# Kernel optimization log

Hardware: AMD Instinct MI355X
Metric: run time of the kernel (lower is better)

The kernel has to match this reference:

```python
import jax, jax.numpy as jnp
import numpy as np

D_CONV = 4  # matches Mamba(d_conv=4)


def _silu(v):
    return v * jax.nn.sigmoid(v)


def _mamba_block(x, in_w, cw, cb, xw, dtw, dtb, A_log, Dp, ow):
    # x: (B, L, d_model)
    B, L, _ = x.shape
    d_inner, d_state = A_log.shape
    xz = x @ in_w.T                        # (B, L, 2*d_inner)
    xr, z = jnp.split(xz, 2, axis=-1)      # each (B, L, d_inner)
    # causal depthwise conv1d (pad d_conv-1 on the left, truncate to L)
    xp = jnp.pad(xr, ((0, 0), (D_CONV - 1, 0), (0, 0)))
    xc = sum(xp[:, k:k + L, :] * cw[:, k] for k in range(D_CONV)) + cb
    xc = _silu(xc)                         # (B, L, d_inner)
    dbl = xc @ xw.T                        # (B, L, dt_rank + 2*d_state)
    dt_rank = dbl.shape[-1] - 2 * d_state
    dt, Bm, Cm = jnp.split(dbl, [dt_rank, dt_rank + d_state], axis=-1)
    dt = jax.nn.softplus(dt @ dtw.T + dtb)  # (B, L, d_inner)
    A = -jnp.exp(A_log)                    # (d_inner, d_state)
    dA = jnp.exp(dt[..., None] * A)                          # (B, L, d_inner, d_state)
    dBx = dt[..., None] * Bm[:, :, None, :] * xc[..., None]  # (B, L, d_inner, d_state)

    def step(h, inputs):
        dA_t, dBx_t, C_t = inputs          # (B,d,s), (B,d,s), (B,s)
        h = dA_t * h + dBx_t
        y = jnp.einsum('bds,bs->bd', h, C_t)
        return h, y

    h0 = jnp.zeros((B, d_inner, d_state), x.dtype)
    _, ys = jax.lax.scan(step, h0, (dA.transpose(1, 0, 2, 3),
                                    dBx.transpose(1, 0, 2, 3),
                                    Cm.transpose(1, 0, 2)))
    y = ys.transpose(1, 0, 2) + xc * Dp    # skip term D*u
    y = y * _silu(z)                       # gated
    return y @ ow.T                        # (B, L, d_model)


def setup_inputs() -> dict:
    key = jax.random.key(0)
    d_model, d_state, n_layer = 1024, 16, 2
    d_inner = 2 * d_model
    dt_rank = d_model // 16  # ceil(1024/16)
    Bsz, L = 2, 1024
    ks = jax.random.split(key, 8)
    s = 0.02
    x = jax.random.normal(ks[0], (Bsz, L, d_model), jnp.float32)
    in_proj_w = jax.random.normal(ks[1], (n_layer, 2 * d_inner, d_model), jnp.float32) * s
    conv_w = jax.random.normal(ks[2], (n_layer, d_inner, D_CONV), jnp.float32) * 0.2
    conv_b = jnp.zeros((n_layer, d_inner), jnp.float32)
    x_proj_w = jax.random.normal(ks[3], (n_layer, dt_rank + 2 * d_state, d_inner), jnp.float32) * s
    dt_proj_w = jax.random.normal(ks[4], (n_layer, d_inner, dt_rank), jnp.float32) * s
    dt_proj_b = jax.random.uniform(ks[5], (n_layer, d_inner), jnp.float32, -5.0, -3.0)
    A_log = jnp.log(jnp.tile(jnp.arange(1, d_state + 1, dtype=jnp.float32), (n_layer, d_inner, 1)))
    D = jnp.ones((n_layer, d_inner), jnp.float32)
    out_proj_w = jax.random.normal(ks[6], (n_layer, d_model, d_inner), jnp.float32) * s
    return {"x": x, "in_proj_w": in_proj_w, "conv_w": conv_w, "conv_b": conv_b,
            "x_proj_w": x_proj_w, "dt_proj_w": dt_proj_w, "dt_proj_b": dt_proj_b,
            "A_log": A_log, "D": D, "out_proj_w": out_proj_w}


def reference(x, in_proj_w, conv_w, conv_b, x_proj_w, dt_proj_w, dt_proj_b, A_log, D, out_proj_w):
    n_layer = in_proj_w.shape[0]
    for i in range(n_layer):
        x = _mamba_block(x, in_proj_w[i], conv_w[i], conv_b[i], x_proj_w[i],
                         dt_proj_w[i], dt_proj_b[i], A_log[i], D[i], out_proj_w[i])
    return x
```

## Files before the change

kernel.cpp:

```cpp
#include <hip/hip_runtime.h>
#include <hip/hip_bf16.h>
#include <cmath>

typedef __bf16 bf16x8_t __attribute__((ext_vector_type(8)));
typedef float  f32x4_t  __attribute__((ext_vector_type(4)));
using bf16 = __hip_bfloat16;

#define LOG2E 1.44269504088896340736f
#define LN2   0.69314718055994530942f

#define AS1C(p) ((const __attribute__((address_space(1))) void*)(p))
#define AS3C(p) ((__attribute__((address_space(3))) void*)(p))

__device__ __forceinline__ float fexp2(float x) { return __builtin_amdgcn_exp2f(x); }
__device__ __forceinline__ float flog2(float x) { return __builtin_amdgcn_logf(x); }
__device__ __forceinline__ float frcp (float x) { return __builtin_amdgcn_rcpf(x); }

__global__ __launch_bounds__(256)
void cast_multi(const float* s0, bf16* d0, int e0,
                const float* s1, bf16* d1, int e1,
                const float* s2, bf16* d2, int e2,
                const float* s3, bf16* d3, int e3,
                const float* s4, bf16* d4, int e4)
{
    const int blk = blockIdx.x;
    const float* src; bf16* dst; int base;
    if      (blk < e0) { src = s0; dst = d0; base = blk; }
    else if (blk < e1) { src = s1; dst = d1; base = blk - e0; }
    else if (blk < e2) { src = s2; dst = d2; base = blk - e1; }
    else if (blk < e3) { src = s3; dst = d3; base = blk - e2; }
    else               { src = s4; dst = d4; base = blk - e3; }

    const int i = base * 256 + threadIdx.x;
    const float4* s = (const float4*)(src + (size_t)i * 8);
    float4 a = s[0], b = s[1];
    bf16 o[8];
    o[0] = __float2bfloat16(a.x); o[1] = __float2bfloat16(a.y);
    o[2] = __float2bfloat16(a.z); o[3] = __float2bfloat16(a.w);
    o[4] = __float2bfloat16(b.x); o[5] = __float2bfloat16(b.y);
    o[6] = __float2bfloat16(b.z); o[7] = __float2bfloat16(b.w);
    *(int4*)(dst + (size_t)i * 8) = *(int4*)o;
}

template<int MODE, bool SPLITK>
__global__ __launch_bounds__(256)
void gemm_bf16(const bf16* __restrict__ A, const bf16* __restrict__ B,
               float* __restrict__ Cf, bf16* __restrict__ Cb,
               int M, int N, int K, int lda, int ldb, int ldc)
{
    __shared__ __align__(16) bf16 At[2][128][32];
    __shared__ __align__(16) bf16 Bt[2][128][32];

    const int tid  = threadIdx.x;
    const int lane = tid & 63;
    const int wid  = tid >> 6;
    const int wr   = wid >> 1;
    const int wc   = wid & 1;
    const int fr   = lane & 15;
    const int fq   = lane >> 4;

    const int row0 = blockIdx.y * 128;
    const int col0 = blockIdx.x * 128;
    const int kb   = SPLITK ? blockIdx.z * K : 0;

    const int g_row = wid * 32 + (lane >> 2);
    const int g_kp  = (lane & 3) * 8;
    const bf16* aP0 = A + (size_t)(row0 + g_row) * lda + g_kp + kb;
    const bf16* aP1 = A + (size_t)(row0 + g_row + 16) * lda + g_kp + kb;
    int bR0 = col0 + g_row;      if (bR0 >= N) bR0 = N - 1;
    int bR1 = col0 + g_row + 16; if (bR1 >= N) bR1 = N - 1;
    const bf16* bP0 = B + (size_t)bR0 * ldb + g_kp + kb;
    const bf16* bP1 = B + (size_t)bR1 * ldb + g_kp + kb;

    f32x4_t acc[4][4];
    #pragma unroll
    for (int m = 0; m < 4; ++m)
        #pragma unroll
        for (int n = 0; n < 4; ++n)
            acc[m][n] = f32x4_t{0.f, 0.f, 0.f, 0.f};

    auto STAGE = [&](int buf, int k0) {
        __builtin_amdgcn_global_load_lds(AS1C(aP0 + k0), AS3C(&At[buf][wid * 32][0]),      16, 0, 0);
        __builtin_amdgcn_global_load_lds(AS1C(aP1 + k0), AS3C(&At[buf][wid * 32 + 16][0]), 16, 0, 0);
        __builtin_amdgcn_global_load_lds(AS1C(bP0 + k0), AS3C(&Bt[buf][wid * 32][0]),      16, 0, 0);
        __builtin_amdgcn_global_load_lds(AS1C(bP1 + k0), AS3C(&Bt[buf][wid * 32 + 16][0]), 16, 0, 0);
    };

    STAGE(0, 0);
    __syncthreads();
    int cur = 0;
    for (int k0 = 0; k0 < K; k0 += 32) {
        if (k0 + 32 < K) STAGE(cur ^ 1, k0 + 32);

        bf16x8_t af[4], bg[4];
        #pragma unroll
        for (int m = 0; m < 4; ++m)
            af[m] = *(const bf16x8_t*)&At[cur][wr * 64 + m * 16 + fr][fq * 8];
        #pragma unroll
        for (int n = 0; n < 4; ++n)
            bg[n] = *(const bf16x8_t*)&Bt[cur][wc * 64 + n * 16 + fr][fq * 8];
        #pragma unroll
        for (int m = 0; m < 4; ++m)
            #pragma unroll
            for (int n = 0; n < 4; ++n)
                acc[m][n] = __builtin_amdgcn_mfma_f32_16x16x32_bf16(
                    af[m], bg[n], acc[m][n], 0, 0, 0);

        __syncthreads();
        cur ^= 1;
    }

    float* Cfz = SPLITK ? (Cf + (size_t)blockIdx.z * M * ldc) : Cf;

    #pragma unroll
    for (int m = 0; m < 4; ++m) {
        #pragma unroll
        for (int n = 0; n < 4; ++n) {
            const int c = col0 + wc * 64 + n * 16 + fr;
            if (c < N) {
                #pragma unroll
                for (int r = 0; r < 4; ++r) {
                    const int rr = row0 + wr * 64 + m * 16 + fq * 4 + r;
                    if (SPLITK || MODE != 1) Cfz[(size_t)rr * ldc + c] = acc[m][n][r];
                    if (!SPLITK && MODE != 0) Cb[(size_t)rr * ldc + c] = __float2bfloat16(acc[m][n][r]);
                }
            }
        }
    }
}

__global__ __launch_bounds__(256)
void reduce_pk(const float* __restrict__ part, float* __restrict__ of,
               bf16* __restrict__ oh, int n4, int stride4, int S)
{
    const int i = blockIdx.x * blockDim.x + threadIdx.x;
    if (i >= n4) return;
    const float4* p4 = (const float4*)part;
    float4 s = p4[i];
    for (int k = 1; k < S; ++k) {
        float4 v = p4[(size_t)k * stride4 + i];
        s.x += v.x; s.y += v.y; s.z += v.z; s.w += v.w;
    }
    if (of) ((float4*)of)[i] = s;
    if (oh) {
        bf16 o[4];
        o[0] = __float2bfloat16(s.x); o[1] = __float2bfloat16(s.y);
        o[2] = __float2bfloat16(s.z); o[3] = __float2bfloat16(s.w);
        *(int2*)(oh + (size_t)i * 4) = *(int2*)o;
    }
}

__global__ __launch_bounds__(256)
void conv_silu(const bf16* __restrict__ xz, const float* __restrict__ cw,
               const float* __restrict__ cb, bf16* __restrict__ xc,
               int Bsz, int L, int dinner)
{
    const int nv = dinner / 4;
    const int g  = blockIdx.x * blockDim.x + threadIdx.x;
    const int d4 = (g % nv) * 4;
    const int t  = (g / nv) % L;
    const int b  = g / (nv * L);
    if (b >= Bsz) return;

    const int ldxz = 2 * dinner;
    float4 w0 = *(const float4*)(cw + (size_t)(d4 + 0) * 4);
    float4 w1 = *(const float4*)(cw + (size_t)(d4 + 1) * 4);
    float4 w2 = *(const float4*)(cw + (size_t)(d4 + 2) * 4);
    float4 w3 = *(const float4*)(cw + (size_t)(d4 + 3) * 4);
    float4 acc = *(const float4*)(cb + d4);

    const bf16* base = xz + (size_t)b * L * ldxz + d4;
    #pragma unroll
    for (int k = 0; k < 4; ++k) {
        const int ts = t - 3 + k;
        if (ts >= 0) {
            const bf16* rp = base + (size_t)ts * ldxz;
            float vx = __bfloat162float(rp[0]);
            float vy = __bfloat162float(rp[1]);
            float vz = __bfloat162float(rp[2]);
            float vw = __bfloat162float(rp[3]);
            acc.x = fmaf(vx, (&w0.x)[k], acc.x);
            acc.y = fmaf(vy, (&w1.x)[k], acc.y);
            acc.z = fmaf(vz, (&w2.x)[k], acc.z);
            acc.w = fmaf(vw, (&w3.x)[k], acc.w);
        }
    }
    acc.x = acc.x * frcp(1.f + fexp2(-acc.x * LOG2E));
    acc.y = acc.y * frcp(1.f + fexp2(-acc.y * LOG2E));
    acc.z = acc.z * frcp(1.f + fexp2(-acc.z * LOG2E));
    acc.w = acc.w * frcp(1.f + fexp2(-acc.w * LOG2E));

    bf16 o[4];
    o[0] = __float2bfloat16(acc.x); o[1] = __float2bfloat16(acc.y);
    o[2] = __float2bfloat16(acc.z); o[3] = __float2bfloat16(acc.w);
    *(int2*)(xc + ((size_t)b * L + t) * dinner + d4) = *(int2*)o;
}

__global__ __launch_bounds__(256)
void scan_part1(const bf16* __restrict__ dtraw, const bf16* __restrict__ xc,
                const float* __restrict__ dbl, const float* __restrict__ dtb,
                const float* __restrict__ alog, float* __restrict__ hend,
                float* __restrict__ Ssum, int Bsz, int L, int dinner,
                int NC, int CL)
{
    const int g  = blockIdx.x * blockDim.x + threadIdx.x;
    const int sq = g & 3;
    const int d  = (g >> 2) % dinner;
    const int c  = ((g >> 2) / dinner) % NC;
    const int b  = g / (4 * dinner * NC);
    if (b >= Bsz) return;

    float4 av = *(const float4*)(alog + (size_t)d * 16 + sq * 4);
    const float As0 = -fexp2(av.x * LOG2E) * LOG2E;
    const float As1 = -fexp2(av.y * LOG2E) * LOG2E;
    const float As2 = -fexp2(av.z * LOG2E) * LOG2E;
    const float As3 = -fexp2(av.w * LOG2E) * LOG2E;
    const float bias = dtb[d];

    const int t0 = c * CL;
    const bf16*  dt_p = dtraw + ((size_t)b * L + t0) * dinner + d;
    const bf16*  xc_p = xc    + ((size_t)b * L + t0) * dinner + d;
    const float* bl_p = dbl   + ((size_t)b * L + t0) * 96 + 64 + sq * 4;

    float h0 = 0.f, h1 = 0.f, h2 = 0.f, h3 = 0.f, S = 0.f;
    for (int t = 0; t < CL; ++t) {
        const float dtv = __bfloat162float(*dt_p);
        const float xcv = __bfloat162float(*xc_p);
        const float4 Bv = *(const float4*)bl_p;

        const float xv = dtv + bias;
        const float e  = fexp2(xv * LOG2E);
        const float sp = (xv > 15.f) ? xv : LN2 * flog2(1.f + e);
        S += sp;
        const float u = sp * xcv;
        h0 = fmaf(fexp2(sp * As0), h0, u * Bv.x);
        h1 = fmaf(fexp2(sp * As1), h1, u * Bv.y);
        h2 = fmaf(fexp2(sp * As2), h2, u * Bv.z);
        h3 = fmaf(fexp2(sp * As3), h3, u * Bv.w);

        dt_p += dinner; xc_p += dinner; bl_p += 96;
    }

    const size_t idx = ((size_t)b * NC + c) * dinner + d;
    *(float4*)(hend + idx * 16 + sq * 4) = make_float4(h0, h1, h2, h3);
    if (sq == 0) Ssum[idx] = S;
}

__global__ __launch_bounds__(256)
void scan_part2(bf16* dty, const bf16* __restrict__ xc,
                const float* __restrict__ dbl, const bf16* __restrict__ xz,
                const float* __restrict__ dtb, const float* __restrict__ alog,
                const float* __restrict__ Dp, const float* __restrict__ hend,
                const float* __restrict__ Ssum,
                int Bsz, int L, int dinner, int NC, int CL)
{
    const int g  = blockIdx.x * blockDim.x + threadIdx.x;
    const int sq = g & 3;
    const int d  = (g >> 2) % dinner;
    const int c  = ((g >> 2) / dinner) % NC;
    const int b  = g / (4 * dinner * NC);
    if (b >= Bsz) return;

    float4 av = *(const float4*)(alog + (size_t)d * 16 + sq * 4);
    const float As0 = -fexp2(av.x * LOG2E) * LOG2E;
    const float As1 = -fexp2(av.y * LOG2E) * LOG2E;
    const float As2 = -fexp2(av.z * LOG2E) * LOG2E;
    const float As3 = -fexp2(av.w * LOG2E) * LOG2E;
    const float bias = dtb[d];
    const float Dval = Dp[d];

    float h0 = 0.f, h1 = 0.f, h2 = 0.f, h3 = 0.f;
    for (int cp = 0; cp < c; ++cp) {
        const size_t idx = ((size_t)b * NC + cp) * dinner + d;
        const float4 he = *(const float4*)(hend + idx * 16 + sq * 4);
        const float  Sv = Ssum[idx];
        h0 = fmaf(fexp2(As0 * Sv), h0, he.x);
        h1 = fmaf(fexp2(As1 * Sv), h1, he.y);
        h2 = fmaf(fexp2(As2 * Sv), h2, he.z);
        h3 = fmaf(fexp2(As3 * Sv), h3, he.w);
    }

    const int t0 = c * CL;
    bf16*        dt_p = dty + ((size_t)b * L + t0) * dinner + d;
    const bf16*  xc_p = xc  + ((size_t)b * L + t0) * dinner + d;
    const float* bl_p = dbl + ((size_t)b * L + t0) * 96 + 64 + sq * 4;
    const bf16*  z_p  = xz  + ((size_t)b * L + t0) * (2 * dinner) + dinner + d;

    for (int t = 0; t < CL; ++t) {
        const float dtv = __bfloat162float(*dt_p);
        const float xcv = __bfloat162float(*xc_p);
        const float4 Bv = *(const float4*)bl_p;
        const float4 Cv = *(const float4*)(bl_p + 16);
        const float zv  = __bfloat162float(*z_p);

        const float xv = dtv + bias;
        const float e  = fexp2(xv * LOG2E);
        const float sp = (xv > 15.f) ? xv : LN2 * flog2(1.f + e);
        const float u = sp * xcv;
        h0 = fmaf(fexp2(sp * As0), h0, u * Bv.x);
        h1 = fmaf(fexp2(sp * As1), h1, u * Bv.y);
        h2 = fmaf(fexp2(sp * As2), h2, u * Bv.z);
        h3 = fmaf(fexp2(sp * As3), h3, u * Bv.w);

        float y = h0 * Cv.x + h1 * Cv.y + h2 * Cv.z + h3 * Cv.w;
        y += __shfl_xor(y, 1, 4);
        y += __shfl_xor(y, 2, 4);

        if (sq == 0) {
            y = fmaf(xcv, Dval, y);
            const float sig = frcp(1.f + fexp2(-zv * LOG2E));
            *dt_p = __float2bfloat16(y * (zv * sig));
        }

        dt_p += dinner; xc_p += dinner; bl_p += 96; z_p += 2 * dinner;
    }
}

extern "C" void kernel_launch(void* const* d_in, const int* in_sizes, int n_in,
                              void* d_out, int out_size, void* d_ws, size_t ws_size,
                              hipStream_t stream)
{
    const float* x    = (const float*)d_in[0];
    const float* inw  = (const float*)d_in[1];
    const float* cw   = (const float*)d_in[2];
    const float* cb   = (const float*)d_in[3];
    const float* xw   = (const float*)d_in[4];
    const float* dtw  = (const float*)d_in[5];
    const float* dtb  = (const float*)d_in[6];
    const float* alog = (const float*)d_in[7];
    const float* Dp   = (const float*)d_in[8];
    const float* ow   = (const float*)d_in[9];
    float* out = (float*)d_out;

    const int Bsz = 2, L = 1024, dmodel = 1024, dinner = 2048;
    const int BL = Bsz * L;
    const int NC = 32, CL = L / NC;
    const int SPX = 16, KSX = dinner / SPX;
    const int SPO = 2,  KSO = dinner / SPO;

    char* p = (char*)d_ws;
    auto alloc = [&](size_t bytes) { char* r = p; p += (bytes + 63) & ~size_t(63); return r; };
    bf16*  wb_in  = (bf16*) alloc((size_t)2 * 2 * dinner * dmodel * 2);
    bf16*  wb_x   = (bf16*) alloc((size_t)2 * 96 * dinner * 2);
    bf16*  wb_dt  = (bf16*) alloc((size_t)2 * dinner * 64 * 2);
    bf16*  wb_ow  = (bf16*) alloc((size_t)2 * dmodel * dinner * 2);
    bf16*  curb   = (bf16*) alloc((size_t)BL * dmodel * 2);
    bf16*  xzb16  = (bf16*) alloc((size_t)BL * 2 * dinner * 2);
    bf16*  xcb16  = (bf16*) alloc((size_t)BL * dinner * 2);
    float* dblb   = (float*)alloc((size_t)BL * 96 * 4);
    bf16*  dblb16 = (bf16*) alloc((size_t)BL * 96 * 2);
    bf16*  dtrb16 = (bf16*) alloc((size_t)BL * dinner * 2);
    float* hendb  = (float*)alloc((size_t)Bsz * NC * dinner * 16 * 4);
    float* ssumb  = (float*)alloc((size_t)Bsz * NC * dinner * 4);
    float* partb  = (float*)alloc((size_t)SPO * BL * dmodel * 4);

    const int scan_blocks = (Bsz * NC * dinner * 4) / 256;

    {
        const int n8_x  = BL * dmodel / 8;
        const int n8_in = 2 * 2 * dinner * dmodel / 8;
        const int n8_xw = 2 * 96 * dinner / 8;
        const int n8_dt = 2 * dinner * 64 / 8;
        const int n8_ow = 2 * dmodel * dinner / 8;
        const int e0 = n8_x / 256;
        const int e1 = e0 + n8_in / 256;
        const int e2 = e1 + n8_xw / 256;
        const int e3 = e2 + n8_dt / 256;
        const int e4 = e3 + n8_ow / 256;
        cast_multi<<<e4, 256, 0, stream>>>(
            x, curb, e0, inw, wb_in, e1, xw, wb_x, e2, dtw, wb_dt, e3, ow, wb_ow, e4);
    }

    for (int l = 0; l < 2; ++l) {
        const bf16*  wb_in_l = wb_in + (size_t)l * 2 * dinner * dmodel;
        const bf16*  wb_x_l  = wb_x  + (size_t)l * 96 * dinner;
        const bf16*  wb_dt_l = wb_dt + (size_t)l * dinner * 64;
        const bf16*  wb_ow_l = wb_ow + (size_t)l * dmodel * dinner;
        const float* cw_l    = cw   + (size_t)l * dinner * 4;
        const float* cb_l    = cb   + (size_t)l * dinner;
        const float* dtb_l   = dtb  + (size_t)l * dinner;
        const float* alog_l  = alog + (size_t)l * dinner * 16;
        const float* Dp_l    = Dp   + (size_t)l * dinner;

        gemm_bf16<1, false><<<dim3(2 * dinner / 128, BL / 128), 256, 0, stream>>>(
            curb, wb_in_l, nullptr, xzb16, BL, 2 * dinner, dmodel, dmodel, dmodel, 2 * dinner);

        conv_silu<<<(BL * dinner / 4) / 256, 256, 0, stream>>>(
            xzb16, cw_l, cb_l, xcb16, Bsz, L, dinner);

        gemm_bf16<0, true><<<dim3(1, BL / 128, SPX), 256, 0, stream>>>(
            xcb16, wb_x_l, partb, nullptr, BL, 96, KSX, dinner, dinner, 96);
        reduce_pk<<<(BL * 96 / 4 + 255) / 256, 256, 0, stream>>>(
            partb, dblb, dblb16, BL * 96 / 4, BL * 96 / 4, SPX);

        gemm_bf16<1, false><<<dim3(dinner / 128, BL / 128), 256, 0, stream>>>(
            dblb16, wb_dt_l, nullptr, dtrb16, BL, dinner, 64, 96, 64, dinner);

        scan_part1<<<scan_blocks, 256, 0, stream>>>(
            dtrb16, xcb16, dblb, dtb_l, alog_l, hendb, ssumb, Bsz, L, dinner, NC, CL);
        scan_part2<<<scan_blocks, 256, 0, stream>>>(
            dtrb16, xcb16, dblb, xzb16, dtb_l, alog_l, Dp_l, hendb, ssumb,
            Bsz, L, dinner, NC, CL);

        gemm_bf16<0, true><<<dim3(dmodel / 128, BL / 128, SPO), 256, 0, stream>>>(
            dtrb16, wb_ow_l, partb, nullptr, BL, dmodel, KSO, dinner, dinner, dmodel);
        if (l == 0)
            reduce_pk<<<(BL * dmodel / 4 + 255) / 256, 256, 0, stream>>>(
                partb, nullptr, curb, BL * dmodel / 4, BL * dmodel / 4, SPO);
        else
            reduce_pk<<<(BL * dmodel / 4 + 255) / 256, 256, 0, stream>>>(
                partb, out, nullptr, BL * dmodel / 4, BL * dmodel / 4, SPO);
    }
}
```

Before: 331.4 us.

## Swizzle GEMM LDS tiles and add separate chunk-prefix kernel for scan

Two changes. First, the bf16 GEMM's LDS layout gets an XOR swizzle on the 8-element k-chunk, applied both where global_load_lds writes and where MFMA fragments are read, so LDS bank conflicts drop. Second, each scan_part2 thread used to walk every preceding chunk's end state itself, which is quadratic work in the chunk count. A new chunk_prefix kernel now computes the exclusive prefix of chunk states once and writes it in place over hend, and scan_part2 reads its initial state directly. This costs an extra kernel launch and a serial pass over NC per (b,d,s) lane.

```diff
diff --git a/kernel.cpp b/kernel.cpp
--- a/kernel.cpp
+++ b/kernel.cpp
@@ -64,7 +64,7 @@
     const int kb   = SPLITK ? blockIdx.z * K : 0;
 
     const int g_row = wid * 32 + (lane >> 2);
-    const int g_kp  = (lane & 3) * 8;
+    const int g_kp  = (((lane & 3) ^ ((lane >> 3) & 3)) * 8);
     const bf16* aP0 = A + (size_t)(row0 + g_row) * lda + g_kp + kb;
     const bf16* aP1 = A + (size_t)(row0 + g_row + 16) * lda + g_kp + kb;
     int bR0 = col0 + g_row;      if (bR0 >= N) bR0 = N - 1;
@@ -72,6 +72,8 @@
     const bf16* bP0 = B + (size_t)bR0 * ldb + g_kp + kb;
     const bf16* bP1 = B + (size_t)bR1 * ldb + g_kp + kb;
 
+    const int rchunk = (fq ^ ((fr >> 1) & 3)) * 8;
+
     f32x4_t acc[4][4];
     #pragma unroll
     for (int m = 0; m < 4; ++m)
@@ -95,10 +97,10 @@
         bf16x8_t af[4], bg[4];
         #pragma unroll
         for (int m = 0; m < 4; ++m)
-            af[m] = *(const bf16x8_t*)&At[cur][wr * 64 + m * 16 + fr][fq * 8];
+            af[m] = *(const bf16x8_t*)&At[cur][wr * 64 + m * 16 + fr][rchunk];
         #pragma unroll
         for (int n = 0; n < 4; ++n)
-            bg[n] = *(const bf16x8_t*)&Bt[cur][wc * 64 + n * 16 + fr][fq * 8];
+            bg[n] = *(const bf16x8_t*)&Bt[cur][wc * 64 + n * 16 + fr][rchunk];
         #pragma unroll
         for (int m = 0; m < 4; ++m)
             #pragma unroll
@@ -247,11 +249,32 @@
 }
 
 __global__ __launch_bounds__(256)
+void chunk_prefix(float* __restrict__ hend, const float* __restrict__ Ssum,
+                  const float* __restrict__ alog, int Bsz, int dinner, int NC)
+{
+    const int g = blockIdx.x * blockDim.x + threadIdx.x;
+    const int s = g & 15;
+    const int d = (g >> 4) % dinner;
+    const int b = g / (16 * dinner);
+    if (b >= Bsz) return;
+
+    const float As2 = -fexp2(alog[(size_t)d * 16 + s] * LOG2E) * LOG2E;
+
+    float h = 0.f;
+    for (int c = 0; c < NC; ++c) {
+        const size_t idx = ((size_t)b * NC + c) * dinner + d;
+        const float he = hend[idx * 16 + s];
+        const float Sv = Ssum[idx];
+        hend[idx * 16 + s] = h;
+        h = fmaf(fexp2(As2 * Sv), h, he);
+    }
+}
+
+__global__ __launch_bounds__(256)
 void scan_part2(bf16* dty, const bf16* __restrict__ xc,
                 const float* __restrict__ dbl, const bf16* __restrict__ xz,
                 const float* __restrict__ dtb, const float* __restrict__ alog,
-                const float* __restrict__ Dp, const float* __restrict__ hend,
-                const float* __restrict__ Ssum,
+                const float* __restrict__ Dp, const float* __restrict__ hinit,
                 int Bsz, int L, int dinner, int NC, int CL)
 {
     const int g  = blockIdx.x * blockDim.x + threadIdx.x;
@@ -269,16 +292,9 @@
     const float bias = dtb[d];
     const float Dval = Dp[d];
 
-    float h0 = 0.f, h1 = 0.f, h2 = 0.f, h3 = 0.f;
-    for (int cp = 0; cp < c; ++cp) {
-        const size_t idx = ((size_t)b * NC + cp) * dinner + d;
-        const float4 he = *(const float4*)(hend + idx * 16 + sq * 4);
-        const float  Sv = Ssum[idx];
-        h0 = fmaf(fexp2(As0 * Sv), h0, he.x);
-        h1 = fmaf(fexp2(As1 * Sv), h1, he.y);
-        h2 = fmaf(fexp2(As2 * Sv), h2, he.z);
-        h3 = fmaf(fexp2(As3 * Sv), h3, he.w);
-    }
+    const size_t cidx = ((size_t)b * NC + c) * dinner + d;
+    float4 hv = *(const float4*)(hinit + cidx * 16 + sq * 4);
+    float h0 = hv.x, h1 = hv.y, h2 = hv.z, h3 = hv.w;
 
     const int t0 = c * CL;
     bf16*        dt_p = dty + ((size_t)b * L + t0) * dinner + d;
@@ -355,6 +371,7 @@
     float* partb  = (float*)alloc((size_t)SPO * BL * dmodel * 4);
 
     const int scan_blocks = (Bsz * NC * dinner * 4) / 256;
+    const int pfx_blocks  = (Bsz * dinner * 16) / 256;
 
     {
         const int n8_x  = BL * dmodel / 8;
@@ -398,8 +415,10 @@
 
         scan_part1<<<scan_blocks, 256, 0, stream>>>(
             dtrb16, xcb16, dblb, dtb_l, alog_l, hendb, ssumb, Bsz, L, dinner, NC, CL);
+        chunk_prefix<<<pfx_blocks, 256, 0, stream>>>(
+            hendb, ssumb, alog_l, Bsz, dinner, NC);
         scan_part2<<<scan_blocks, 256, 0, stream>>>(
-            dtrb16, xcb16, dblb, xzb16, dtb_l, alog_l, Dp_l, hendb, ssumb,
+            dtrb16, xcb16, dblb, xzb16, dtb_l, alog_l, Dp_l, hendb,
             Bsz, L, dinner, NC, CL);
 
         gemm_bf16<0, true><<<dim3(dmodel / 128, BL / 128, SPO), 256, 0, stream>>>(
```

Result: no change. 332.6 us (+0.4%).
